# Kernel tuning notes

Measured on AMD Instinct MI355X. Metric: run time of the kernel, lower is better.

## Reference

```python
import jax, jax.numpy as jnp
import numpy as np

B, S = 1, 4096
H, KV, D, HID = 8, 4, 256, 2304   # heads, kv heads, head_dim, hidden_size
G = H // KV                        # GQA group size
WINDOW = 1024                      # sliding window
THETA = 10000.0                    # rope_local_base_freq (sliding attention)
EPS = 1e-6
SCALE = 256.0 ** -0.5              # query_pre_attn_scalar ** -0.5


def rms_norm(x, w, eps=EPS):
    # Gemma3RMSNorm: fp32 rms over last dim, scale by (1 + weight)
    v = jnp.mean(jnp.square(x), axis=-1, keepdims=True)
    return x * jax.lax.rsqrt(v + eps) * (1.0 + w)


def rope(x, position_ids):
    # x: [B, S, N, D]; split-half rotation as in Gemma3RotaryEmbedding
    d = x.shape[-1]
    inv_freq = 1.0 / (THETA ** (jnp.arange(0, d, 2, dtype=jnp.float32) / d))  # [D/2]
    freqs = position_ids.astype(jnp.float32)[:, :, None] * inv_freq  # [B, S, D/2]
    cos = jnp.cos(freqs)[:, :, None, :]  # [B, S, 1, D/2]
    sin = jnp.sin(freqs)[:, :, None, :]
    x1, x2 = jnp.split(x, 2, axis=-1)
    return jnp.concatenate([x1 * cos - x2 * sin, x1 * sin + x2 * cos], axis=-1)


def setup_inputs() -> dict:
    key = jax.random.key(0)
    ks = jax.random.split(key, 6)
    n = lambda k, shp, sc: jax.random.normal(k, shp, dtype=jnp.float32) * sc
    return {
        "x": n(ks[0], (B, S, HID), 1.0),
        "position_ids": jnp.broadcast_to(jnp.arange(S, dtype=jnp.int32)[None, :], (B, S)),
        "wq": n(ks[1], (HID, H * D), 0.02),
        "wk": n(ks[2], (HID, KV * D), 0.02),
        "wv": n(ks[3], (HID, KV * D), 0.02),
        "wo": n(ks[4], (H * D, HID), 0.02),
        "q_norm_w": jnp.zeros((D,), dtype=jnp.float32),
        "k_norm_w": jnp.zeros((D,), dtype=jnp.float32),
    }


def reference(x, position_ids, wq, wk, wv, wo, q_norm_w, k_norm_w):
    b, s, _ = x.shape
    q = (x @ wq).reshape(b, s, H, D)
    k = (x @ wk).reshape(b, s, KV, D)
    v = (x @ wv).reshape(b, s, KV, D)

    # QK-RMSNorm over head_dim, then RoPE, then query scaling
    q = rms_norm(q, q_norm_w)
    k = rms_norm(k, k_norm_w)
    q = rope(q, position_ids)
    k = rope(k, position_ids)
    q = q * SCALE

    # GQA: group queries over shared KV heads. qg: [B, S, KV, G, D]
    qg = q.reshape(b, s, KV, G, D)
    scores = jnp.einsum('bqcgd,btcd->bcgqt', qg, k)  # [B, KV, G, S, S]

    # causal + sliding-window mask: t <= q and q - t < WINDOW
    pi = position_ids[:, :, None]  # query positions [B, S, 1]
    pj = position_ids[:, None, :]  # key positions   [B, 1, S]
    mask = (pj <= pi) & (pi - pj < WINDOW)  # [B, S, S]
    neg = jnp.finfo(scores.dtype).min
    scores = jnp.where(mask[:, None, None, :, :], scores, neg)

    probs = jax.nn.softmax(scores, axis=-1)
    out = jnp.einsum('bcgqt,btcd->bqcgd', probs, v).reshape(b, s, H * D)
    return out @ wo
```

## Files before the change

### kernel.cpp

```cpp
#include <hip/hip_runtime.h>
#include <stdint.h>

typedef unsigned short u16;
typedef __attribute__((ext_vector_type(8))) short bf16x8;
typedef __attribute__((ext_vector_type(4))) float f32x4;

#define S_LEN 4096
#define HID_DIM 2304
#define QKV_N 4096
#define AO_N 2048
#define HD 256
#define WIN 1024
#define QSCALE 0.0625f

static __device__ __forceinline__ u16 f2bf(float f) {
  union { float f; uint32_t u; } v; v.f = f;
  return (u16)((v.u + 0x7FFFu + ((v.u >> 16) & 1u)) >> 16);
}
static __device__ __forceinline__ float bf2f(u16 h) {
  union { uint32_t u; float f; } v; v.u = ((uint32_t)h) << 16;
  return v.f;
}

static __device__ __forceinline__ void gld16(const void* src, void* dst) {
  __builtin_amdgcn_global_load_lds((const __attribute__((address_space(1))) void*)src,
                                   (__attribute__((address_space(3))) void*)dst, 16, 0, 0);
}

#define BAR() __builtin_amdgcn_s_barrier()
#define LG0() asm volatile("s_waitcnt lgkmcnt(0)" ::: "memory")
#define VM6() asm volatile("s_waitcnt vmcnt(6)" ::: "memory")
#define VM5() asm volatile("s_waitcnt vmcnt(5)" ::: "memory")
#define VM4() asm volatile("s_waitcnt vmcnt(4)" ::: "memory")
#define VM3() asm volatile("s_waitcnt vmcnt(3)" ::: "memory")
#define VM2() asm volatile("s_waitcnt vmcnt(2)" ::: "memory")
#define VM0() asm volatile("s_waitcnt vmcnt(0)" ::: "memory")
#define PRIO1() __builtin_amdgcn_s_setprio(1)
#define PRIO0() __builtin_amdgcn_s_setprio(0)

__global__ __launch_bounds__(256) void k_cvt_bf16(const float* __restrict__ in,
                                                  u16* __restrict__ out, int n) {
  int i = (blockIdx.x * 256 + threadIdx.x) * 4;
  if (i >= n) return;
  float4 v = *(const float4*)(in + i);
  uint64_t p = (uint64_t)f2bf(v.x) | ((uint64_t)f2bf(v.y) << 16)
             | ((uint64_t)f2bf(v.z) << 32) | ((uint64_t)f2bf(v.w) << 48);
  *(uint64_t*)(out + i) = p;
}

__global__ __launch_bounds__(256) void k_transpose_cvt(const float* __restrict__ in, int C,
                                                       u16* __restrict__ out, int out_stride,
                                                       int row_off) {
  __shared__ float tile[32][33];
  int c0 = blockIdx.x * 32, r0 = blockIdx.y * 32;
  int tx = threadIdx.x & 31, ty = threadIdx.x >> 5;
#pragma unroll
  for (int i = 0; i < 4; i++)
    tile[ty + i * 8][tx] = in[(size_t)(r0 + ty + i * 8) * C + c0 + tx];
  __syncthreads();
#pragma unroll
  for (int i = 0; i < 4; i++)
    out[(size_t)(row_off + c0 + ty + i * 8) * out_stride + r0 + tx] = f2bf(tile[tx][ty + i * 8]);
}

__global__ __launch_bounds__(256) void k_transpose_w(const float* __restrict__ wq,
                                                     const float* __restrict__ wk,
                                                     const float* __restrict__ wv,
                                                     u16* __restrict__ out) {
  int ct = blockIdx.x;
  int r0 = blockIdx.y * 32;
  const float* src;
  int C, c0;
  if (ct < 64) {
    src = wq; C = 2048; c0 = ct * 32;
  } else if (ct < 96) {
    src = wk; C = 1024; c0 = (ct - 64) * 32;
  } else {
    src = wv; C = 1024; c0 = (ct - 96) * 32;
  }
  __shared__ float tile[32][33];
  int tx = threadIdx.x & 31, ty = threadIdx.x >> 5;
#pragma unroll
  for (int i = 0; i < 4; i++)
    tile[ty + i * 8][tx] = src[(size_t)(r0 + ty + i * 8) * C + c0 + tx];
  __syncthreads();
#pragma unroll
  for (int i = 0; i < 4; i++)
    out[(size_t)(ct * 32 + ty + i * 8) * HID_DIM + r0 + tx] = f2bf(tile[tx][ty + i * 8]);
}

__global__ __launch_bounds__(256) void k_vtrans(const u16* __restrict__ qkv,
                                                u16* __restrict__ vtout) {
  __shared__ u16 tile[32][33];
  int c0 = blockIdx.x * 32, s0 = blockIdx.y * 32;
  int tx = threadIdx.x & 31, ty = threadIdx.x >> 5;
#pragma unroll
  for (int i = 0; i < 4; i++)
    tile[ty + i * 8][tx] = qkv[(size_t)(s0 + ty + i * 8) * QKV_N + 3072 + c0 + tx];
  __syncthreads();
#pragma unroll
  for (int i = 0; i < 4; i++)
    vtout[(size_t)(c0 + ty + i * 8) * S_LEN + s0 + tx] = tile[tx][ty + i * 8];
}

template <int OUT_BF16>
__global__ __launch_bounds__(512, 2) void k_gemm8p(const u16* __restrict__ A,
                                                   const u16* __restrict__ Bt,
                                                   void* __restrict__ Cout,
                                                   int M, int N, int K) {
  __shared__ u16 sA[2][256 * 64];
  __shared__ u16 sB[2][256 * 64];
  const int t = threadIdx.x, lane = t & 63, wave = t >> 6;
  const int wr = wave >> 2, wc = wave & 3;
  const int l15 = lane & 15, l4 = lane >> 4;
  const int nbn = N >> 8;
  const int cpx = gridDim.x >> 3;
  const int wg = ((int)blockIdx.x & 7) * cpx + ((int)blockIdx.x >> 3);
  const int bm = wg / nbn, bn = wg % nbn;
  const int NT = K >> 6;
  const int srow = lane >> 3;
  const int sslot = ((lane & 7) ^ srow) * 8;
  const u16* Abase = A + (size_t)(bm * 256) * K;
  const u16* Bbase = Bt + (size_t)(bn * 256) * K;
  f32x4 acc[8][4] = {};
  bf16x8 aF[4][2], b01[2][2], b23[2][2];

#define STG_A(BUF, HALF, KT) do {                                                 \
    _Pragma("unroll")                                                             \
    for (int c_ = 0; c_ < 2; c_++) {                                              \
      int rb_ = (HALF) * 128 + (wave * 2 + c_) * 8;                               \
      gld16(Abase + (size_t)(rb_ + srow) * K + ((KT) << 6) + sslot,               \
            &sA[BUF][rb_ * 64]);                                                  \
    }                                                                             \
  } while (0)
#define STG_B(BUF, HALF, KT) do {                                                 \
    _Pragma("unroll")                                                             \
    for (int c_ = 0; c_ < 2; c_++) {                                              \
      int rb_ = (HALF) * 128 + (wave * 2 + c_) * 8;                               \
      gld16(Bbase + (size_t)(rb_ + srow) * K + ((KT) << 6) + sslot,               \
            &sB[BUF][rb_ * 64]);                                                  \
    }                                                                             \
  } while (0)
#define LDA(BUF, M_, KK)                                                          \
  (*(const bf16x8*)&sA[BUF][((M_) * 32 + wr * 16 + l15) * 64 +                    \
                            ((((KK) << 2) + l4) ^ (l15 & 7)) * 8])
#define LDB(BUF, N_, KK)                                                          \
  (*(const bf16x8*)&sB[BUF][((N_) * 64 + wc * 16 + l15) * 64 +                    \
                            ((((KK) << 2) + l4) ^ (l15 & 7)) * 8])

#define P1_LOADS(b_) do {                                                         \
    _Pragma("unroll") for (int m_ = 0; m_ < 4; m_++)                              \
      _Pragma("unroll") for (int k_ = 0; k_ < 2; k_++)                            \
        aF[m_][k_] = LDA(b_, m_, k_);                                             \
    _Pragma("unroll") for (int n_ = 0; n_ < 2; n_++)                              \
      _Pragma("unroll") for (int k_ = 0; k_ < 2; k_++)                            \
        b01[n_][k_] = LDB(b_, n_, k_);                                            \
  } while (0)
#define P2_LOADS(b_) do {                                                         \
    _Pragma("unroll") for (int n_ = 0; n_ < 2; n_++)                              \
      _Pragma("unroll") for (int k_ = 0; k_ < 2; k_++)                            \
        b23[n_][k_] = LDB(b_, n_ + 2, k_);                                        \
  } while (0)
#define P3_LOADS(b_) do {                                                         \
    _Pragma("unroll") for (int m_ = 0; m_ < 4; m_++)                              \
      _Pragma("unroll") for (int k_ = 0; k_ < 2; k_++)                            \
        aF[m_][k_] = LDA(b_, m_ + 4, k_);                                         \
  } while (0)
#define MFMA16(MOFF, NOFF, BREG) do {                                             \
    _Pragma("unroll") for (int m_ = 0; m_ < 4; m_++)                              \
      _Pragma("unroll") for (int n_ = 0; n_ < 2; n_++)                            \
        _Pragma("unroll") for (int k_ = 0; k_ < 2; k_++)                          \
          acc[m_ + MOFF][n_ + NOFF] = __builtin_amdgcn_mfma_f32_16x16x32_bf16(    \
              aF[m_][k_], BREG[n_][k_], acc[m_ + MOFF][n_ + NOFF], 0, 0, 0);      \
  } while (0)

  STG_A(0, 0, 0);
  STG_B(0, 0, 0);
  STG_B(0, 1, 0);
  STG_A(0, 1, 0);
  VM4();
  BAR();

  for (int tt = 0; tt < NT - 1; ++tt) {
    const int b = tt & 1, nb = b ^ 1;
    P1_LOADS(b);
    STG_A(nb, 0, tt + 1);
    STG_B(nb, 0, tt + 1);
    BAR(); LG0(); PRIO1(); MFMA16(0, 0, b01); PRIO0();
    VM6();
    BAR();
    P2_LOADS(b);
    STG_B(nb, 1, tt + 1);
    BAR(); LG0(); PRIO1(); MFMA16(0, 2, b23); PRIO0();
    VM6();
    BAR();
    P3_LOADS(b);
    STG_A(nb, 1, tt + 1);
    BAR(); LG0(); PRIO1(); MFMA16(4, 0, b01); PRIO0();
    BAR();
    PRIO1(); MFMA16(4, 2, b23); PRIO0();
    VM4();
    BAR();
  }
  {
    const int b = (NT - 1) & 1;
    P1_LOADS(b);
    BAR(); LG0(); PRIO1(); MFMA16(0, 0, b01); PRIO0();
    VM2();
    BAR();
    P2_LOADS(b);
    BAR(); LG0(); PRIO1(); MFMA16(0, 2, b23); PRIO0();
    VM0();
    BAR();
    P3_LOADS(b);
    BAR(); LG0(); PRIO1(); MFMA16(4, 0, b01); PRIO0();
    BAR();
    PRIO1(); MFMA16(4, 2, b23); PRIO0();
  }

#pragma unroll
  for (int m = 0; m < 8; m++)
#pragma unroll
    for (int n = 0; n < 4; n++)
#pragma unroll
      for (int r = 0; r < 4; r++) {
        size_t row = bm * 256 + m * 32 + wr * 16 + l4 * 4 + r;
        size_t col = bn * 256 + n * 64 + wc * 16 + l15;
        if (OUT_BF16)
          ((u16*)Cout)[row * N + col] = f2bf(acc[m][n][r]);
        else
          ((float*)Cout)[row * N + col] = acc[m][n][r];
      }
#undef STG_A
#undef STG_B
#undef LDA
#undef LDB
#undef P1_LOADS
#undef P2_LOADS
#undef P3_LOADS
#undef MFMA16
}

__global__ __launch_bounds__(512, 2) void k_gemm192(const u16* __restrict__ A,
                                                    const u16* __restrict__ Bt,
                                                    float* __restrict__ Cout,
                                                    int M, int N, int K) {
  __shared__ u16 sA[2][256 * 64];
  __shared__ u16 sB[2][192 * 64];
  const int t = threadIdx.x, lane = t & 63, wave = t >> 6;
  const int wr = wave >> 2, wc = wave & 3;
  const int l15 = lane & 15, l4 = lane >> 4;
  const int nbn = N / 192;
  const int cpx = gridDim.x >> 3;
  const int wg = ((int)blockIdx.x & 7) * cpx + ((int)blockIdx.x >> 3);
  const int bm = wg / nbn, bn = wg % nbn;
  const int NT = K >> 6;
  const int srow = lane >> 3;
  const int sslot = ((lane & 7) ^ srow) * 8;
  const u16* Abase = A + (size_t)(bm * 256) * K;
  const u16* Bbase = Bt + (size_t)(bn * 192) * K;
  f32x4 acc[8][3] = {};
  bf16x8 aF[4][2], b01[2][2], b2[2];

#define GA_STG_A(BUF, HALF, KT) do {                                              \
    _Pragma("unroll")                                                             \
    for (int c_ = 0; c_ < 2; c_++) {                                              \
      int rb_ = (HALF) * 128 + (wave * 2 + c_) * 8;                               \
      gld16(Abase + (size_t)(rb_ + srow) * K + ((KT) << 6) + sslot,               \
            &sA[BUF][rb_ * 64]);                                                  \
    }                                                                             \
  } while (0)
#define GA_STG_BC(BUF, CH, KT) do {                                               \
    int rb_ = (CH) * 64 + wave * 8;                                               \
    gld16(Bbase + (size_t)(rb_ + srow) * K + ((KT) << 6) + sslot,                 \
          &sB[BUF][rb_ * 64]);                                                    \
  } while (0)
#define GA_LDA(BUF, M_, KK)                                                       \
  (*(const bf16x8*)&sA[BUF][((M_) * 32 + wr * 16 + l15) * 64 +                    \
                            ((((KK) << 2) + l4) ^ (l15 & 7)) * 8])
#define GA_LDB(BUF, N_, KK)                                                       \
  (*(const bf16x8*)&sB[BUF][((N_) * 64 + wc * 16 + l15) * 64 +                    \
                            ((((KK) << 2) + l4) ^ (l15 & 7)) * 8])
#define GA_P1_LOADS(b_) do {                                                      \
    _Pragma("unroll") for (int m_ = 0; m_ < 4; m_++)                              \
      _Pragma("unroll") for (int k_ = 0; k_ < 2; k_++)                            \
        aF[m_][k_] = GA_LDA(b_, m_, k_);                                          \
    _Pragma("unroll") for (int n_ = 0; n_ < 2; n_++)                              \
      _Pragma("unroll") for (int k_ = 0; k_ < 2; k_++)                            \
        b01[n_][k_] = GA_LDB(b_, n_, k_);                                         \
  } while (0)
#define GA_P2_LOADS(b_) do {                                                      \
    _Pragma("unroll") for (int k_ = 0; k_ < 2; k_++)                              \
      b2[k_] = GA_LDB(b_, 2, k_);                                                 \
  } while (0)
#define GA_P3_LOADS(b_) do {                                                      \
    _Pragma("unroll") for (int m_ = 0; m_ < 4; m_++)                              \
      _Pragma("unroll") for (int k_ = 0; k_ < 2; k_++)                            \
        aF[m_][k_] = GA_LDA(b_, m_ + 4, k_);                                      \
  } while (0)
#define GA_MFMA_N01(MOFF) do {                                                    \
    _Pragma("unroll") for (int m_ = 0; m_ < 4; m_++)                              \
      _Pragma("unroll") for (int n_ = 0; n_ < 2; n_++)                            \
        _Pragma("unroll") for (int k_ = 0; k_ < 2; k_++)                          \
          acc[m_ + MOFF][n_] = __builtin_amdgcn_mfma_f32_16x16x32_bf16(           \
              aF[m_][k_], b01[n_][k_], acc[m_ + MOFF][n_], 0, 0, 0);              \
  } while (0)
#define GA_MFMA_N2(MOFF) do {                                                     \
    _Pragma("unroll") for (int m_ = 0; m_ < 4; m_++)                              \
      _Pragma("unroll") for (int k_ = 0; k_ < 2; k_++)                            \
        acc[m_ + MOFF][2] = __builtin_amdgcn_mfma_f32_16x16x32_bf16(              \
            aF[m_][k_], b2[k_], acc[m_ + MOFF][2], 0, 0, 0);                      \
  } while (0)

  GA_STG_A(0, 0, 0);
  GA_STG_BC(0, 0, 0);
  GA_STG_BC(0, 1, 0);
  GA_STG_BC(0, 2, 0);
  GA_STG_A(0, 1, 0);
  VM3();
  BAR();

  for (int tt = 0; tt < NT - 1; ++tt) {
    const int b = tt & 1, nb = b ^ 1;
    GA_P1_LOADS(b);
    GA_STG_A(nb, 0, tt + 1);
    GA_STG_BC(nb, 0, tt + 1);
    GA_STG_BC(nb, 1, tt + 1);
    BAR(); LG0(); PRIO1(); GA_MFMA_N01(0); PRIO0();
    VM6();
    BAR();
    GA_P2_LOADS(b);
    GA_STG_BC(nb, 2, tt + 1);
    BAR(); LG0(); PRIO1(); GA_MFMA_N2(0); PRIO0();
    VM5();
    BAR();
    GA_P3_LOADS(b);
    GA_STG_A(nb, 1, tt + 1);
    BAR(); LG0(); PRIO1(); GA_MFMA_N01(4); PRIO0();
    BAR();
    PRIO1(); GA_MFMA_N2(4); PRIO0();
    VM3();
    BAR();
  }
  {
    const int b = (NT - 1) & 1;
    GA_P1_LOADS(b);
    BAR(); LG0(); PRIO1(); GA_MFMA_N01(0); PRIO0();
    VM2();
    BAR();
    GA_P2_LOADS(b);
    BAR(); LG0(); PRIO1(); GA_MFMA_N2(0); PRIO0();
    VM0();
    BAR();
    GA_P3_LOADS(b);
    BAR(); LG0(); PRIO1(); GA_MFMA_N01(4); PRIO0();
    BAR();
    PRIO1(); GA_MFMA_N2(4); PRIO0();
  }

#pragma unroll
  for (int m = 0; m < 8; m++)
#pragma unroll
    for (int n = 0; n < 3; n++)
#pragma unroll
      for (int r = 0; r < 4; r++) {
        size_t row = bm * 256 + m * 32 + wr * 16 + l4 * 4 + r;
        size_t col = bn * 192 + n * 64 + wc * 16 + l15;
        Cout[row * N + col] = acc[m][n][r];
      }
#undef GA_STG_A
#undef GA_STG_BC
#undef GA_LDA
#undef GA_LDB
#undef GA_P1_LOADS
#undef GA_P2_LOADS
#undef GA_P3_LOADS
#undef GA_MFMA_N01
#undef GA_MFMA_N2
}

__global__ __launch_bounds__(128) void k_normrope(u16* __restrict__ qkv,
                                                  const int* __restrict__ pos_ids,
                                                  const float* __restrict__ qw,
                                                  const float* __restrict__ kw) {
  __shared__ float cross[2];
  int idx = blockIdx.x;
  int s = idx / 12, r = idx % 12;
  bool is_q = (r < 8);
  u16* p = qkv + (size_t)s * QKV_N + (is_q ? r * HD : 2048 + (r - 8) * HD);
  const float* w = is_q ? qw : kw;
  int j = threadIdx.x;
  float x1 = bf2f(p[j]), x2 = bf2f(p[j + 128]);
  float ss = x1 * x1 + x2 * x2;
#pragma unroll
  for (int off = 1; off < 64; off <<= 1) ss += __shfl_xor(ss, off);
  if ((threadIdx.x & 63) == 0) cross[threadIdx.x >> 6] = ss;
  __syncthreads();
  float rms = rsqrtf((cross[0] + cross[1]) * (1.0f / 256.0f) + 1e-6f);
  float y1 = x1 * rms * (1.0f + w[j]);
  float y2 = x2 * rms * (1.0f + w[j + 128]);
  float ang = (float)pos_ids[s] * exp2f((float)j * (-13.287712379549449f / 128.0f));
  float sn, c;
  sincosf(ang, &sn, &c);
  float sc = is_q ? QSCALE : 1.0f;
  p[j] = f2bf((y1 * c - y2 * sn) * sc);
  p[j + 128] = f2bf((y1 * sn + y2 * c) * sc);
}

__global__ __launch_bounds__(512, 2) void k_attn(const u16* __restrict__ qkv,
                                                 const u16* __restrict__ vt,
                                                 const int* __restrict__ pos_ids,
                                                 u16* __restrict__ aout) {
  __shared__ u16 lK[2][64 * 256];
  __shared__ u16 lV[2][256 * 64];
  __shared__ u16 lP[8][16 * 64];
  const int bid = blockIdx.x;
  const int wg = (bid & 7) * 32 + (bid >> 3);
  const int kvh = wg >> 6;
  const int q0 = (wg & 63) * 64;
  const int t = threadIdx.x, lane = t & 63, wave = t >> 6;
  const int l15 = lane & 15, l4 = lane >> 4;
  const int head = kvh * 2 + (wave >> 2);
  const int qw = q0 + (wave & 3) * 16;

  bf16x8 qfr[8];
  {
    const u16* qptr = qkv + (size_t)(qw + l15) * QKV_N + head * HD + l4 * 8;
#pragma unroll
    for (int kc = 0; kc < 8; kc++) qfr[kc] = *(const bf16x8*)(qptr + kc * 32);
  }
  f32x4 acc[16] = {};
  float mrow[4], lrow[4];
#pragma unroll
  for (int r = 0; r < 4; r++) { mrow[r] = -1e30f; lrow[r] = 0.0f; }
  int qi[4];
#pragma unroll
  for (int r = 0; r < 4; r++) qi[r] = pos_ids[qw + l4 * 4 + r];

  const int krw = lane >> 5, kcl = lane & 31;
  const int vrw = lane >> 3, vcl = lane & 7;
  const u16* kgb = qkv + 2048 + kvh * HD;
  const u16* vgb = vt + (size_t)kvh * HD * S_LEN;

  int start = q0 - (WIN - 1);
  if (start < 0) start = 0;
  start &= ~63;

#define STAGE_KV(B, T0) do {                                                          \
    _Pragma("unroll")                                                                 \
    for (int i_ = 0; i_ < 4; i_++) {                                                  \
      int ch_ = wave * 4 + i_;                                                        \
      int kr_ = ch_ * 2 + krw;                                                        \
      gld16(kgb + (size_t)((T0) + kr_) * QKV_N + ((kcl ^ (kr_ & 7)) * 8),             \
            &lK[B][ch_ * 512]);                                                       \
      int vr_ = ch_ * 8 + vrw;                                                        \
      gld16(vgb + (size_t)vr_ * S_LEN + (T0) + ((vcl ^ (vr_ & 7)) * 8),               \
            &lV[B][ch_ * 512]);                                                       \
    }                                                                                 \
  } while (0)

  STAGE_KV(0, start);
  __syncthreads();
  int buf = 0;
  for (int t0 = start; t0 <= q0 + 63; t0 += 64) {
    if (t0 + 64 <= q0 + 63) STAGE_KV(buf ^ 1, t0 + 64);
    int kp[4];
#pragma unroll
    for (int kb = 0; kb < 4; kb++) kp[kb] = pos_ids[t0 + kb * 16 + l15];
    f32x4 sv[4] = {};
    PRIO1();
#pragma unroll
    for (int kb = 0; kb < 4; kb++) {
      const char* krow = (const char*)&lK[buf][(kb * 16 + l15) * 256];
      const int sw = ((kb * 16 + l15) & 7) << 4;
#pragma unroll
      for (int kc = 0; kc < 8; kc++) {
        bf16x8 kf = *(const bf16x8*)(krow + ((kc * 64 + l4 * 16) ^ sw));
        sv[kb] = __builtin_amdgcn_mfma_f32_16x16x32_bf16(qfr[kc], kf, sv[kb], 0, 0, 0);
      }
    }
    PRIO0();
    float sloc[4][4], mx[4];
    float need = 0.0f;
#pragma unroll
    for (int r = 0; r < 4; r++) {
      int pi = qi[r];
#pragma unroll
      for (int kb = 0; kb < 4; kb++)
        sloc[r][kb] = ((kp[kb] <= pi) && (pi - kp[kb] < WIN)) ? sv[kb][r] : -__builtin_inff();
      float m_ = fmaxf(fmaxf(sloc[r][0], sloc[r][1]), fmaxf(sloc[r][2], sloc[r][3]));
#pragma unroll
      for (int off = 1; off < 16; off <<= 1) m_ = fmaxf(m_, __shfl_xor(m_, off));
      mx[r] = m_;
      need = fmaxf(need, m_ - mrow[r]);
    }
    bool resc = __any(need > 8.0f);
    if (resc) {
#pragma unroll
      for (int r = 0; r < 4; r++) {
        float nm = fmaxf(mrow[r], mx[r]);
        float al = __expf(mrow[r] - nm);
        mrow[r] = nm;
        lrow[r] *= al;
#pragma unroll
        for (int nd = 0; nd < 16; nd++) acc[nd][r] *= al;
      }
    }
#pragma unroll
    for (int r = 0; r < 4; r++) {
      float nm = mrow[r];
      float e0 = __expf(sloc[r][0] - nm), e1 = __expf(sloc[r][1] - nm);
      float e2 = __expf(sloc[r][2] - nm), e3 = __expf(sloc[r][3] - nm);
      float sum = (e0 + e1) + (e2 + e3);
#pragma unroll
      for (int off = 1; off < 16; off <<= 1) sum += __shfl_xor(sum, off);
      lrow[r] += sum;
      int q = l4 * 4 + r;
      char* lpw = (char*)&lP[wave][0] + q * 128;
      int swp = (q & 7) << 4;
      *(u16*)(lpw + ((l15 * 2) ^ swp)) = f2bf(e0);
      *(u16*)(lpw + ((32 + l15 * 2) ^ swp)) = f2bf(e1);
      *(u16*)(lpw + ((64 + l15 * 2) ^ swp)) = f2bf(e2);
      *(u16*)(lpw + ((96 + l15 * 2) ^ swp)) = f2bf(e3);
    }
#pragma unroll
    for (int kc2 = 0; kc2 < 2; kc2++) {
      int q = l15;
      bf16x8 pa = *(const bf16x8*)((const char*)&lP[wave][0] + q * 128 +
                                   ((kc2 * 64 + l4 * 16) ^ ((q & 7) << 4)));
      PRIO1();
#pragma unroll
      for (int nd = 0; nd < 16; nd++) {
        int d = nd * 16 + l15;
        bf16x8 vf = *(const bf16x8*)((const char*)&lV[buf][d * 64] +
                                     ((kc2 * 64 + l4 * 16) ^ ((d & 7) << 4)));
        acc[nd] = __builtin_amdgcn_mfma_f32_16x16x32_bf16(pa, vf, acc[nd], 0, 0, 0);
      }
      PRIO0();
    }
    __syncthreads();
    buf ^= 1;
  }
  float rinv[4];
#pragma unroll
  for (int r = 0; r < 4; r++) rinv[r] = 1.0f / lrow[r];
#pragma unroll
  for (int nd = 0; nd < 16; nd++)
#pragma unroll
    for (int r = 0; r < 4; r++) {
      size_t row = qw + l4 * 4 + r;
      aout[row * AO_N + head * HD + nd * 16 + l15] = f2bf(acc[nd][r] * rinv[r]);
    }
#undef STAGE_KV
}

extern "C" void kernel_launch(void* const* d_in, const int* in_sizes, int n_in,
                              void* d_out, int out_size, void* d_ws, size_t ws_size,
                              hipStream_t stream) {
  const float* x = (const float*)d_in[0];
  const int* pos = (const int*)d_in[1];
  const float* wq = (const float*)d_in[2];
  const float* wk = (const float*)d_in[3];
  const float* wv = (const float*)d_in[4];
  const float* wo = (const float*)d_in[5];
  const float* qnw = (const float*)d_in[6];
  const float* knw = (const float*)d_in[7];

  u16* qkv = (u16*)d_out;
  u16* xbf = (u16*)d_ws;
  u16* wT = (u16*)((char*)d_ws + 18874368);
  u16* vtb = (u16*)((char*)d_ws + 28311552);
  u16* aout = xbf;

  k_cvt_bf16<<<9216, 256, 0, stream>>>(x, xbf, S_LEN * HID_DIM);
  k_transpose_w<<<dim3(128, 72), 256, 0, stream>>>(wq, wk, wv, wT);
  k_gemm8p<1><<<dim3(256), 512, 0, stream>>>(xbf, wT, qkv, S_LEN, QKV_N, HID_DIM);
  k_vtrans<<<dim3(32, 128), 256, 0, stream>>>(qkv, vtb);
  k_normrope<<<S_LEN * 12, 128, 0, stream>>>(qkv, pos, qnw, knw);
  k_transpose_cvt<<<dim3(72, 64), 256, 0, stream>>>(wo, HID_DIM, wT, 2048, 0);
  k_attn<<<dim3(256), 512, 0, stream>>>(qkv, vtb, pos, aout);
  k_gemm192<<<dim3(192), 512, 0, stream>>>(aout, wT, (float*)d_out, S_LEN, HID_DIM, 2048);
}
```

Measured before the change: 243.2 us.

## Fuse QK RMSNorm, RoPE and V transpose into the QKV GEMM epilogue

Drops the separate k_vtrans and k_normrope kernels. The QKV GEMM epilogue now stages each 32-row accumulator slab in LDS, applies RMSNorm, RoPE and the query scale for Q/K column tiles, and writes V out transposed into the vt buffer directly. A small new kernel precomputes the cos/sin tables into spare output memory. This removes two kernel launches and a round trip of the bf16 QKV through global memory, at the cost of extra LDS staging and barriers in the GEMM epilogue and extra reads of the cos/sin tables.

```diff
diff --git a/kernel.cpp b/kernel.cpp
--- a/kernel.cpp
+++ b/kernel.cpp
@@ -46,6 +46,18 @@
   uint64_t p = (uint64_t)f2bf(v.x) | ((uint64_t)f2bf(v.y) << 16)
              | ((uint64_t)f2bf(v.z) << 32) | ((uint64_t)f2bf(v.w) << 48);
   *(uint64_t*)(out + i) = p;
+}
+
+__global__ __launch_bounds__(256) void k_sincos(const int* __restrict__ pos_ids,
+                                                float* __restrict__ ctab,
+                                                float* __restrict__ stab) {
+  int idx = blockIdx.x * 256 + threadIdx.x;
+  int s = idx >> 7, j = idx & 127;
+  float ang = (float)pos_ids[s] * exp2f((float)j * (-13.287712379549449f / 128.0f));
+  float sn, c;
+  sincosf(ang, &sn, &c);
+  ctab[idx] = c;
+  stab[idx] = sn;
 }
 
 __global__ __launch_bounds__(256) void k_transpose_cvt(const float* __restrict__ in, int C,
@@ -89,25 +101,16 @@
     out[(size_t)(ct * 32 + ty + i * 8) * HID_DIM + r0 + tx] = f2bf(tile[tx][ty + i * 8]);
 }
 
-__global__ __launch_bounds__(256) void k_vtrans(const u16* __restrict__ qkv,
-                                                u16* __restrict__ vtout) {
-  __shared__ u16 tile[32][33];
-  int c0 = blockIdx.x * 32, s0 = blockIdx.y * 32;
-  int tx = threadIdx.x & 31, ty = threadIdx.x >> 5;
-#pragma unroll
-  for (int i = 0; i < 4; i++)
-    tile[ty + i * 8][tx] = qkv[(size_t)(s0 + ty + i * 8) * QKV_N + 3072 + c0 + tx];
-  __syncthreads();
-#pragma unroll
-  for (int i = 0; i < 4; i++)
-    vtout[(size_t)(c0 + ty + i * 8) * S_LEN + s0 + tx] = tile[tx][ty + i * 8];
-}
-
-template <int OUT_BF16>
+template <int MODE>
 __global__ __launch_bounds__(512, 2) void k_gemm8p(const u16* __restrict__ A,
                                                    const u16* __restrict__ Bt,
                                                    void* __restrict__ Cout,
-                                                   int M, int N, int K) {
+                                                   int M, int N, int K,
+                                                   const float* __restrict__ ctab,
+                                                   const float* __restrict__ stab,
+                                                   const float* __restrict__ qnw,
+                                                   const float* __restrict__ knw,
+                                                   u16* __restrict__ vtb) {
   __shared__ u16 sA[2][256 * 64];
   __shared__ u16 sB[2][256 * 64];
   const int t = threadIdx.x, lane = t & 63, wave = t >> 6;
@@ -218,19 +221,83 @@
     PRIO1(); MFMA16(4, 2, b23); PRIO0();
   }
 
-#pragma unroll
-  for (int m = 0; m < 8; m++)
-#pragma unroll
-    for (int n = 0; n < 4; n++)
-#pragma unroll
-      for (int r = 0; r < 4; r++) {
-        size_t row = bm * 256 + m * 32 + wr * 16 + l4 * 4 + r;
-        size_t col = bn * 256 + n * 64 + wc * 16 + l15;
-        if (OUT_BF16)
-          ((u16*)Cout)[row * N + col] = f2bf(acc[m][n][r]);
-        else
+  if (MODE == 1) {
+    __syncthreads();
+    float* slab = (float*)&sA[0][0];
+    if (bn < 12) {
+      const float* wvec = (bn < 8) ? qnw : knw;
+      const float scl = (bn < 8) ? QSCALE : 1.0f;
+      f32x4 wv4 = *(const f32x4*)&wvec[lane * 4];
+#pragma unroll
+      for (int m = 0; m < 8; m++) {
+#pragma unroll
+        for (int n = 0; n < 4; n++)
+#pragma unroll
+          for (int r = 0; r < 4; r++)
+            slab[(wr * 16 + l4 * 4 + r) * 264 + n * 64 + wc * 16 + l15] = acc[m][n][r];
+        __syncthreads();
+#pragma unroll
+        for (int rr = 0; rr < 4; rr++) {
+          int lrow = wave * 4 + rr;
+          int grow = bm * 256 + m * 32 + lrow;
+          f32x4 v = *(const f32x4*)&slab[lrow * 264 + lane * 4];
+          float ss = v[0] * v[0] + v[1] * v[1] + v[2] * v[2] + v[3] * v[3];
+#pragma unroll
+          for (int off = 1; off < 64; off <<= 1) ss += __shfl_xor(ss, off);
+          float rms = rsqrtf(ss * (1.0f / 256.0f) + 1e-6f);
+          float y[4], yo[4];
+#pragma unroll
+          for (int j = 0; j < 4; j++) y[j] = v[j] * rms * (1.0f + wv4[j]);
+#pragma unroll
+          for (int j = 0; j < 4; j++) yo[j] = __shfl_xor(y[j], 32);
+          f32x4 cv = *(const f32x4*)&ctab[grow * 128 + (lane & 31) * 4];
+          f32x4 sv = *(const f32x4*)&stab[grow * 128 + (lane & 31) * 4];
+          uint64_t pk = 0;
+#pragma unroll
+          for (int j = 0; j < 4; j++) {
+            float o = (lane < 32) ? (y[j] * cv[j] - yo[j] * sv[j])
+                                  : (yo[j] * sv[j] + y[j] * cv[j]);
+            pk |= (uint64_t)f2bf(o * scl) << (16 * j);
+          }
+          *(uint64_t*)&((u16*)Cout)[(size_t)grow * N + bn * 256 + lane * 4] = pk;
+        }
+        __syncthreads();
+      }
+    } else {
+      const int kvh = bn - 12;
+      const int d = t >> 1, sh = (t & 1) * 16;
+#pragma unroll
+      for (int m = 0; m < 8; m++) {
+#pragma unroll
+        for (int n = 0; n < 4; n++)
+#pragma unroll
+          for (int r = 0; r < 4; r++)
+            slab[(wr * 16 + l4 * 4 + r) * 264 + n * 64 + wc * 16 + l15] = acc[m][n][r];
+        __syncthreads();
+        u16* dst = vtb + (size_t)(kvh * 256 + d) * S_LEN + bm * 256 + m * 32 + sh;
+#pragma unroll
+        for (int g = 0; g < 4; g++) {
+          uint64_t pk = 0;
+#pragma unroll
+          for (int jj = 0; jj < 4; jj++)
+            pk |= (uint64_t)f2bf(slab[(sh + g * 4 + jj) * 264 + d]) << (16 * jj);
+          *(uint64_t*)(dst + g * 4) = pk;
+        }
+        __syncthreads();
+      }
+    }
+  } else {
+#pragma unroll
+    for (int m = 0; m < 8; m++)
+#pragma unroll
+      for (int n = 0; n < 4; n++)
+#pragma unroll
+        for (int r = 0; r < 4; r++) {
+          size_t row = bm * 256 + m * 32 + wr * 16 + l4 * 4 + r;
+          size_t col = bn * 256 + n * 64 + wc * 16 + l15;
           ((float*)Cout)[row * N + col] = acc[m][n][r];
-      }
+        }
+  }
 #undef STG_A
 #undef STG_B
 #undef LDA
@@ -379,34 +446,6 @@
 #undef GA_MFMA_N2
 }
 
-__global__ __launch_bounds__(128) void k_normrope(u16* __restrict__ qkv,
-                                                  const int* __restrict__ pos_ids,
-                                                  const float* __restrict__ qw,
-                                                  const float* __restrict__ kw) {
-  __shared__ float cross[2];
-  int idx = blockIdx.x;
-  int s = idx / 12, r = idx % 12;
-  bool is_q = (r < 8);
-  u16* p = qkv + (size_t)s * QKV_N + (is_q ? r * HD : 2048 + (r - 8) * HD);
-  const float* w = is_q ? qw : kw;
-  int j = threadIdx.x;
-  float x1 = bf2f(p[j]), x2 = bf2f(p[j + 128]);
-  float ss = x1 * x1 + x2 * x2;
-#pragma unroll
-  for (int off = 1; off < 64; off <<= 1) ss += __shfl_xor(ss, off);
-  if ((threadIdx.x & 63) == 0) cross[threadIdx.x >> 6] = ss;
-  __syncthreads();
-  float rms = rsqrtf((cross[0] + cross[1]) * (1.0f / 256.0f) + 1e-6f);
-  float y1 = x1 * rms * (1.0f + w[j]);
-  float y2 = x2 * rms * (1.0f + w[j + 128]);
-  float ang = (float)pos_ids[s] * exp2f((float)j * (-13.287712379549449f / 128.0f));
-  float sn, c;
-  sincosf(ang, &sn, &c);
-  float sc = is_q ? QSCALE : 1.0f;
-  p[j] = f2bf((y1 * c - y2 * sn) * sc);
-  p[j + 128] = f2bf((y1 * sn + y2 * c) * sc);
-}
-
 __global__ __launch_bounds__(512, 2) void k_attn(const u16* __restrict__ qkv,
                                                  const u16* __restrict__ vt,
                                                  const int* __restrict__ pos_ids,
@@ -567,16 +606,18 @@
   const float* knw = (const float*)d_in[7];
 
   u16* qkv = (u16*)d_out;
+  float* ctab = (float*)((char*)d_out + 33554432);
+  float* stab = (float*)((char*)d_out + 35651584);
   u16* xbf = (u16*)d_ws;
   u16* wT = (u16*)((char*)d_ws + 18874368);
   u16* vtb = (u16*)((char*)d_ws + 28311552);
   u16* aout = xbf;
 
   k_cvt_bf16<<<9216, 256, 0, stream>>>(x, xbf, S_LEN * HID_DIM);
+  k_sincos<<<2048, 256, 0, stream>>>(pos, ctab, stab);
   k_transpose_w<<<dim3(128, 72), 256, 0, stream>>>(wq, wk, wv, wT);
-  k_gemm8p<1><<<dim3(256), 512, 0, stream>>>(xbf, wT, qkv, S_LEN, QKV_N, HID_DIM);
-  k_vtrans<<<dim3(32, 128), 256, 0, stream>>>(qkv, vtb);
-  k_normrope<<<S_LEN * 12, 128, 0, stream>>>(qkv, pos, qnw, knw);
+  k_gemm8p<1><<<dim3(256), 512, 0, stream>>>(xbf, wT, qkv, S_LEN, QKV_N, HID_DIM,
+                                             ctab, stab, qnw, knw, vtb);
   k_transpose_cvt<<<dim3(72, 64), 256, 0, stream>>>(wo, HID_DIM, wT, 2048, 0);
   k_attn<<<dim3(256), 512, 0, stream>>>(qkv, vtb, pos, aout);
   k_gemm192<<<dim3(192), 512, 0, stream>>>(aout, wT, (float*)d_out, S_LEN, HID_DIM, 2048);
```

New measurement: 229.9 us. 1.06x faster.
